# Optimization experiments

Measured on AMD Instinct MI355X. Metric: run time of the kernel, lower is better.

Reference implementation:

```python
import jax, jax.numpy as jnp
import numpy as np

DIM, E, K, H = 512, 8, 2, 16  # hidden_dim is hardcoded to 16 in the torch module
B, N = 8, 4096
BN_EPS = 1e-5


def setup_inputs() -> dict:
    key = jax.random.key(0)
    ks = jax.random.split(key, 12)
    s = 0.02
    return {
        "x": jax.random.normal(ks[0], (B, N, DIM), jnp.float32),
        # gate: Conv1d(dim, dim, 1) -> weight [dim, dim]; BatchNorm1d(dim); Conv1d(dim, E, 1)
        "wg1": jax.random.normal(ks[1], (DIM, DIM), jnp.float32) * s,
        "bg1": jnp.zeros((DIM,), jnp.float32),
        "gamma": jnp.ones((DIM,), jnp.float32),
        "beta": jnp.zeros((DIM,), jnp.float32),
        "wg2": jax.random.normal(ks[2], (E, DIM), jnp.float32) * s,
        "bg2": jnp.zeros((E,), jnp.float32),
        # experts stacked: Linear(dim,16) -> w1 [E, dim, 16]; Linear(16,dim) -> w2 [E, 16, dim]
        "w1": jax.random.normal(ks[3], (E, DIM, H), jnp.float32) * s,
        "b1": jnp.zeros((E, H), jnp.float32),
        "w2": jax.random.normal(ks[4], (E, H, DIM), jnp.float32) * s,
        "b2": jnp.zeros((E, DIM), jnp.float32),
    }


def reference(x, wg1, bg1, gamma, beta, wg2, bg2, w1, b1, w2, b2):
    b, n, c = x.shape
    t = b * n
    flat = x.reshape(t, c)                                 # [T, C]

    # gate: 1x1 conv == per-token linear; BN over all tokens per channel (train-mode batch stats)
    h = flat @ wg1.T + bg1                                  # [T, C]
    mu = h.mean(axis=0)
    var = h.var(axis=0)                                     # biased, matches torch BN normalization
    h = gamma * (h - mu) * jax.lax.rsqrt(var + BN_EPS) + beta
    h = jax.nn.relu(h)
    logits = h @ wg2.T + bg2                                # [T, E]

    vals, idx = jax.lax.top_k(logits, K)                    # [T, K]
    topk_w = jax.nn.softmax(vals, axis=-1)
    weight = jnp.zeros((t, logits.shape[-1]), logits.dtype)
    weight = weight.at[jnp.arange(t)[:, None], idx].set(topk_w)  # scatter, [T, E]

    # dense expert compute for every token (faithful to original)
    h1 = jax.nn.relu(jnp.einsum('tc,ech->teh', flat, w1) + b1)   # [T, E, H]
    all_out = jnp.einsum('teh,ehc->tec', h1, w2) + b2            # [T, E, C]
    out_flat = jnp.einsum('tec,te->tc', all_out, weight)         # masked combine

    out = out_flat.reshape(b, n, c).transpose(0, 2, 1)           # [B, C, N]
    usage = weight.sum(axis=0) / t
    lb_loss = (usage ** 2).sum() * logits.shape[-1]
    return out, lb_loss
```

## Files before the change

kernel.cpp:

```cpp
#include <hip/hip_runtime.h>

#define T_TOK 32768
#define C_DIM 512
#define N_SEQ 4096

typedef unsigned short ushort_t;
typedef unsigned int uint_t;
typedef __attribute__((ext_vector_type(8))) _Float16 half8;
typedef __attribute__((ext_vector_type(4))) float f32x4;

static __device__ __forceinline__ ushort_t f2h_bits(float f) {
  _Float16 h = (_Float16)f;
  return __builtin_bit_cast(ushort_t, h);
}
static __device__ __forceinline__ float h_bits2f(ushort_t u) {
  return (float)__builtin_bit_cast(_Float16, u);
}

static __device__ __forceinline__ half8 frag_ld(const ushort_t* base, int r, int q) {
  const int off = r * 32 + ((q ^ ((r >> 1) & 3)) * 8);
  return *(const half8*)(base + off);
}

#define GLOAD_LDS(gptr, lptr)                                                  \
  __builtin_amdgcn_global_load_lds(                                            \
      (const __attribute__((address_space(1))) uint_t*)(gptr),                 \
      (__attribute__((address_space(3))) uint_t*)(lptr), 16, 0, 0)

__global__ __launch_bounds__(256) void prep(
    const float* __restrict__ X, const float* __restrict__ wg1,
    const float* __restrict__ w1, const float* __restrict__ w2,
    const float* __restrict__ b2, ushort_t* __restrict__ Ahi,
    ushort_t* __restrict__ Alo, ushort_t* __restrict__ Whi,
    ushort_t* __restrict__ Wlo, ushort_t* __restrict__ W1t,
    ushort_t* __restrict__ W2t, float* __restrict__ stats,
    float* __restrict__ usage, uint_t* __restrict__ done) {
  const int idx = blockIdx.x * 256 + threadIdx.x;
  {
    const size_t i0 = (size_t)idx * 8;
    float4 a = *(const float4*)(X + i0);
    float4 b = *(const float4*)(X + i0 + 4);
    float v[8] = {a.x, a.y, a.z, a.w, b.x, b.y, b.z, b.w};
    ushort_t hi[8], lo[8];
#pragma unroll
    for (int j = 0; j < 8; ++j) {
      hi[j] = f2h_bits(v[j]);
      lo[j] = f2h_bits(v[j] - h_bits2f(hi[j]));
    }
    *(uint4*)(Ahi + i0) = *(uint4*)hi;
    *(uint4*)(Alo + i0) = *(uint4*)lo;
  }
  if (blockIdx.x < 1024) {
    {
      const float v = wg1[idx];
      const ushort_t h = f2h_bits(v);
      Whi[idx] = h;
      Wlo[idx] = f2h_bits(v - h_bits2f(h));
    }
    if (idx < 65536) {
      const int eh = idx >> 9, c = idx & 511;
      const int e = eh >> 4, hh = eh & 15;
      W1t[idx] = f2h_bits(w1[((size_t)e * 512 + c) * 16 + hh]);
    }
    if (idx < 81920) {
      const int c = idx / 160, k = idx - c * 160;
      float v = 0.f;
      if (k < 128) {
        const int e = k >> 4, hh = k & 15;
        v = w2[((size_t)e * 16 + hh) * 512 + c];
      } else if (k < 136) {
        v = b2[(size_t)(k - 128) * 512 + c];
      }
      W2t[c * 160 + k] = f2h_bits(v);
    }
  }
  if (blockIdx.x == 4096) {
    float4 z = {0.f, 0.f, 0.f, 0.f};
    *(float4*)&stats[threadIdx.x * 4] = z;
    if (threadIdx.x < 8) usage[threadIdx.x] = 0.f;
    if (threadIdx.x == 8) *done = 0u;
  }
}

__global__ __launch_bounds__(256) void k1_mfma(
    const ushort_t* __restrict__ Ahi, const ushort_t* __restrict__ Alo,
    const ushort_t* __restrict__ Whi, const ushort_t* __restrict__ Wlo,
    const float* __restrict__ bg1, float* __restrict__ H,
    float* __restrict__ stats) {
  __shared__ ushort_t sAh[2][4096], sAl[2][4096];
  const int tid = threadIdx.x, lane = tid & 63, w = tid >> 6;
  const int wm = w >> 1, wn = w & 1;
  const int b = blockIdx.x;
  const int m0 = ((b & 7) | ((b >> 5) << 3)) * 128;
  const int n0 = ((b >> 3) & 3) * 128;
  const int cl = lane & 15, qf = lane >> 4;

  const ushort_t* gA = (w < 2) ? Ahi : Alo;

#define K1_STAGE(kc, buf)                                                      \
  {                                                                            \
    const int k0s = (kc) * 32;                                                 \
    ushort_t* lb = (w < 2) ? sAh[buf] : sAl[buf];                              \
    _Pragma("unroll") for (int j = 0; j < 4; ++j) {                            \
      const int p = j * 128 + (w & 1) * 64 + lane;                             \
      const int r = p >> 2, q = (p & 3) ^ ((r >> 1) & 3);                      \
      GLOAD_LDS(gA + (size_t)(m0 + r) * 512 + k0s + q * 8, lb + p * 8);        \
    }                                                                          \
  }

  f32x4 acc[4][4] = {};
  K1_STAGE(0, 0);

  for (int kc = 0; kc < 16; ++kc) {
    const int k0 = kc * 32;
    __syncthreads();
    if (kc < 15) K1_STAGE(kc + 1, (kc + 1) & 1);

    half8 bh[4], bl[4];
#pragma unroll
    for (int f = 0; f < 4; ++f) {
      const size_t r = (size_t)(n0 + wn * 64 + f * 16 + cl);
      bh[f] = *(const half8*)(Whi + r * 512 + k0 + qf * 8);
      bl[f] = *(const half8*)(Wlo + r * 512 + k0 + qf * 8);
    }
    half8 ah[4], al[4];
    const ushort_t* bAh = sAh[kc & 1];
    const ushort_t* bAl = sAl[kc & 1];
#pragma unroll
    for (int f = 0; f < 4; ++f) {
      ah[f] = frag_ld(bAh, wm * 64 + f * 16 + cl, qf);
      al[f] = frag_ld(bAl, wm * 64 + f * 16 + cl, qf);
    }
#pragma unroll
    for (int i = 0; i < 4; ++i)
#pragma unroll
      for (int j = 0; j < 4; ++j) {
        acc[i][j] = __builtin_amdgcn_mfma_f32_16x16x32_f16(ah[i], bh[j], acc[i][j], 0, 0, 0);
        acc[i][j] = __builtin_amdgcn_mfma_f32_16x16x32_f16(ah[i], bl[j], acc[i][j], 0, 0, 0);
        acc[i][j] = __builtin_amdgcn_mfma_f32_16x16x32_f16(al[i], bh[j], acc[i][j], 0, 0, 0);
      }
  }
#undef K1_STAGE

  float s[4] = {0, 0, 0, 0}, qs[4] = {0, 0, 0, 0};
  const int rq = lane >> 4;
#pragma unroll
  for (int nf = 0; nf < 4; ++nf) {
    const int col = n0 + wn * 64 + nf * 16 + cl;
    const float bv = bg1[col];
#pragma unroll
    for (int mf = 0; mf < 4; ++mf) {
      const int row = m0 + wm * 64 + mf * 16 + rq * 4;
#pragma unroll
      for (int i = 0; i < 4; ++i) {
        const float v = acc[mf][nf][i] + bv;
        H[(size_t)(row + i) * 512 + col] = v;
        s[nf] += v;
        qs[nf] += v * v;
      }
    }
  }
#pragma unroll
  for (int nf = 0; nf < 4; ++nf) {
    s[nf] += __shfl_xor(s[nf], 16, 64);
    qs[nf] += __shfl_xor(qs[nf], 16, 64);
    s[nf] += __shfl_xor(s[nf], 32, 64);
    qs[nf] += __shfl_xor(qs[nf], 32, 64);
  }
  if (lane < 16) {
#pragma unroll
    for (int nf = 0; nf < 4; ++nf) {
      const int col = n0 + wn * 64 + nf * 16 + cl;
      atomicAdd(&stats[col], s[nf]);
      atomicAdd(&stats[512 + col], qs[nf]);
    }
  }
}

__global__ __launch_bounds__(256) void k5_fused(
    const ushort_t* __restrict__ Ahi, const ushort_t* __restrict__ W1t,
    const ushort_t* __restrict__ W2t, const float* __restrict__ b1,
    const float* __restrict__ H, const float* __restrict__ stats,
    const float* __restrict__ gamma, const float* __restrict__ beta,
    const float* __restrict__ wg2, const float* __restrict__ bg2,
    float* __restrict__ usage, uint_t* __restrict__ done,
    float* __restrict__ Out) {
  __shared__ ushort_t sA[2][2048];
  __shared__ ushort_t Pl[64 * 168];
  __shared__ float wtab[64 * 8];
  __shared__ float ys[128 * 68];
  __shared__ float scsh_l[1024];
  __shared__ float lus[8];

  const int tid = threadIdx.x, lane = tid & 63, w = tid >> 6;
  const int wm = w >> 1, wn = w & 1;
  const int t0 = blockIdx.x * 64;
  const int bi = t0 >> 12, n0 = t0 & 4095;
  const int cl = lane & 15, qf = lane >> 4, rq = lane >> 4;

  {
    const int p = tid;
    const int r = p >> 2, q = (p & 3) ^ ((r >> 1) & 3);
    GLOAD_LDS(Ahi + (size_t)(t0 + r) * 512 + q * 8, sA[0] + p * 8);
  }

  if (tid < 8) lus[tid] = 0.f;
  wtab[tid] = 0.f;
  wtab[tid + 256] = 0.f;
  {
    uint4 z = {0, 0, 0, 0};
    const int row = tid >> 2, hf = tid & 3;
    *(uint4*)&Pl[row * 168 + 128 + hf * 8] = z;
  }
#pragma unroll
  for (int rep = 0; rep < 2; ++rep) {
    const int c = tid + rep * 256;
    const double mu = (double)stats[c] * (1.0 / (double)T_TOK);
    const double var = (double)stats[512 + c] * (1.0 / (double)T_TOK) - mu * mu;
    const double rstd = 1.0 / sqrt(var + 1e-5);
    const float scv = (float)((double)gamma[c] * rstd);
    scsh_l[c] = scv;
    scsh_l[512 + c] = beta[c] - (float)mu * scv;
  }
  __syncthreads();

  {
    const int cb = lane * 8;
    float sc[8], sh[8];
#pragma unroll
    for (int i = 0; i < 8; ++i) {
      sc[i] = scsh_l[cb + i];
      sh[i] = scsh_l[512 + cb + i];
    }
    float wg[8][8];
#pragma unroll
    for (int e = 0; e < 8; ++e)
#pragma unroll
      for (int i = 0; i < 8; ++i) wg[e][i] = wg2[e * C_DIM + cb + i];
    float bg[8];
#pragma unroll
    for (int e = 0; e < 8; ++e) bg[e] = bg2[e];

#pragma unroll 2
    for (int it = 0; it < 16; ++it) {
      const int tl = w * 16 + it;
      const float* hr = H + (size_t)(t0 + tl) * C_DIM + cb;
      float4 h0 = *(const float4*)hr;
      float4 h1 = *(const float4*)(hr + 4);
      float y[8] = {h0.x, h0.y, h0.z, h0.w, h1.x, h1.y, h1.z, h1.w};
#pragma unroll
      for (int i = 0; i < 8; ++i) y[i] = fmaxf(fmaf(y[i], sc[i], sh[i]), 0.f);

      float lg[8];
#pragma unroll
      for (int e = 0; e < 8; ++e) {
        float sum = 0.f;
#pragma unroll
        for (int i = 0; i < 8; ++i) sum = fmaf(y[i], wg[e][i], sum);
        lg[e] = sum;
      }
#pragma unroll
      for (int d = 1; d < 64; d <<= 1)
#pragma unroll
        for (int e = 0; e < 8; ++e) lg[e] += __shfl_xor(lg[e], d, 64);
#pragma unroll
      for (int e = 0; e < 8; ++e) lg[e] += bg[e];

      float v1 = lg[0]; int i1 = 0;
#pragma unroll
      for (int e = 1; e < 8; ++e)
        if (lg[e] > v1) { v1 = lg[e]; i1 = e; }
      float v2 = -3.4e38f; int i2 = 0;
#pragma unroll
      for (int e = 0; e < 8; ++e)
        if (e != i1 && lg[e] > v2) { v2 = lg[e]; i2 = e; }

      const float p = expf(v2 - v1);
      const float rw = 1.f / (1.f + p);
      const float w0 = rw, w1 = p * rw;

      if (lane == 0) {
        wtab[tl * 8 + i1] = w0;
        wtab[tl * 8 + i2] = w1;
        Pl[tl * 168 + 128 + i1] = f2h_bits(w0);
        Pl[tl * 168 + 128 + i2] = f2h_bits(w1);
        atomicAdd(&lus[i1], w0);
        atomicAdd(&lus[i2], w1);
      }
    }
  }
  __syncthreads();
  if (tid < 8) atomicAdd(&usage[tid], lus[tid]);
  __syncthreads();
  if (tid == 0) {
    __threadfence();
    const uint_t ticket = atomicAdd(done, 1u);
    if (ticket == 511u) {
      float s = 0.f;
#pragma unroll
      for (int e = 0; e < 8; ++e) {
        const float u = atomicAdd(&usage[e], 0.f) * (1.f / (float)T_TOK);
        s += u * u;
      }
      Out[(size_t)16777216] = s * 8.f;
    }
  }

  f32x4 acc[2][4] = {};
  for (int kc = 0; kc < 16; ++kc) {
    const int k0 = kc * 32;
    __syncthreads();
    if (kc < 15) {
      const int p = tid;
      const int r = p >> 2, q = (p & 3) ^ ((r >> 1) & 3);
      GLOAD_LDS(Ahi + (size_t)(t0 + r) * 512 + (k0 + 32) + q * 8,
                sA[(kc + 1) & 1] + p * 8);
    }
    half8 bf[4];
#pragma unroll
    for (int f = 0; f < 4; ++f)
      bf[f] = *(const half8*)(W1t + (size_t)(wn * 64 + f * 16 + cl) * 512 + k0 + qf * 8);
    half8 af[2];
#pragma unroll
    for (int f = 0; f < 2; ++f) af[f] = frag_ld(sA[kc & 1], wm * 32 + f * 16 + cl, qf);
#pragma unroll
    for (int i = 0; i < 2; ++i)
#pragma unroll
      for (int j = 0; j < 4; ++j)
        acc[i][j] = __builtin_amdgcn_mfma_f32_16x16x32_f16(af[i], bf[j], acc[i][j], 0, 0, 0);
  }

  {
#pragma unroll
    for (int nf = 0; nf < 4; ++nf) {
      const int col = wn * 64 + nf * 16 + cl;
      const float bv = b1[col];
      const int e = wn * 4 + nf;
#pragma unroll
      for (int mf = 0; mf < 2; ++mf) {
        const int row = wm * 32 + mf * 16 + rq * 4;
#pragma unroll
        for (int i = 0; i < 4; ++i) {
          const float v = fmaxf(acc[mf][nf][i] + bv, 0.f) * wtab[(row + i) * 8 + e];
          Pl[(row + i) * 168 + col] = f2h_bits(v);
        }
      }
    }
  }
  __syncthreads();

  for (int nc = 0; nc < 4; ++nc) {
    f32x4 a2[2][4] = {};
#pragma unroll
    for (int kc = 0; kc < 5; ++kc) {
      const int k0 = kc * 32;
      half8 bf4[4];
#pragma unroll
      for (int f = 0; f < 4; ++f)
        bf4[f] = *(const half8*)(W2t + (size_t)(nc * 128 + wn * 64 + f * 16 + cl) * 160 + k0 + qf * 8);
      half8 af[2];
#pragma unroll
      for (int f = 0; f < 2; ++f)
        af[f] = *(const half8*)(Pl + (wm * 32 + f * 16 + cl) * 168 + k0 + qf * 8);
#pragma unroll
      for (int i = 0; i < 2; ++i)
#pragma unroll
        for (int j = 0; j < 4; ++j)
          a2[i][j] = __builtin_amdgcn_mfma_f32_16x16x32_f16(af[i], bf4[j], a2[i][j], 0, 0, 0);
    }
    __syncthreads();
#pragma unroll
    for (int nf = 0; nf < 4; ++nf) {
      const int c = wn * 64 + nf * 16 + cl;
#pragma unroll
      for (int mf = 0; mf < 2; ++mf) {
        const int trow = wm * 32 + mf * 16 + rq * 4;
#pragma unroll
        for (int i = 0; i < 4; ++i) ys[c * 68 + trow + i] = a2[mf][nf][i];
      }
    }
    __syncthreads();
#pragma unroll
    for (int pass = 0; pass < 8; ++pass) {
      const int c = pass * 16 + (tid >> 4);
      const int f4 = tid & 15;
      float4 v = *(const float4*)&ys[c * 68 + f4 * 4];
      *(float4*)&Out[((size_t)(bi * 512 + nc * 128 + c)) * 4096 + n0 + f4 * 4] = v;
    }
  }
}

extern "C" void kernel_launch(void* const* d_in, const int* in_sizes, int n_in,
                              void* d_out, int out_size, void* d_ws, size_t ws_size,
                              hipStream_t stream) {
  const float* x     = (const float*)d_in[0];
  const float* wg1   = (const float*)d_in[1];
  const float* bg1   = (const float*)d_in[2];
  const float* gamma = (const float*)d_in[3];
  const float* beta  = (const float*)d_in[4];
  const float* wg2   = (const float*)d_in[5];
  const float* bg2   = (const float*)d_in[6];
  const float* w1    = (const float*)d_in[7];
  const float* b1    = (const float*)d_in[8];
  const float* w2    = (const float*)d_in[9];
  const float* b2    = (const float*)d_in[10];
  float* out = (float*)d_out;

  char* ws = (char*)d_ws;
  float*    h     = (float*)ws;
  ushort_t* Ahi   = (ushort_t*)(ws + 67108864);
  ushort_t* Alo   = (ushort_t*)(ws + 100663296);
  ushort_t* Whi   = (ushort_t*)(ws + 134217728);
  ushort_t* Wlo   = (ushort_t*)(ws + 134742016);
  ushort_t* W1t   = (ushort_t*)(ws + 135266304);
  ushort_t* W2t   = (ushort_t*)(ws + 135397376);
  float*    stats = (float*)(ws + 135561216);
  float*    usage = (float*)(ws + 135565312);
  uint_t*   done  = (uint_t*)(ws + 135565344);

  prep<<<8192, 256, 0, stream>>>(x, wg1, w1, w2, b2, Ahi, Alo, Whi, Wlo, W1t,
                                 W2t, stats, usage, done);
  k1_mfma<<<1024, 256, 0, stream>>>(Ahi, Alo, Whi, Wlo, bg1, h, stats);
  k5_fused<<<512, 256, 0, stream>>>(Ahi, W1t, W2t, b1, h, stats, gamma, beta,
                                    wg2, bg2, usage, done, out);
}
```

Measured before the change: 288.4 us.

## Fuse fp32-to-fp16 hi/lo split of X into GEMM kernels, drop prep pass

The prep kernel no longer converts X into fp16 hi/lo workspace copies. Instead, k1 and k5 load fp32 X directly into registers, split it into fp16 hi/lo inside the loop, and write the halves to LDS. k1 now also stages the Whi/Wlo tiles into LDS via global_load_lds instead of reading them directly from global memory. This removes a full read and a double-width write of the 64MB activation tensor. The cost is extra conversion ALU work in the GEMMs and an extra barrier per k-step, since k1 no longer double-buffers its LDS.

```diff
diff --git a/kernel.cpp b/kernel.cpp
--- a/kernel.cpp
+++ b/kernel.cpp
@@ -28,53 +28,36 @@
       (__attribute__((address_space(3))) uint_t*)(lptr), 16, 0, 0)
 
 __global__ __launch_bounds__(256) void prep(
-    const float* __restrict__ X, const float* __restrict__ wg1,
-    const float* __restrict__ w1, const float* __restrict__ w2,
-    const float* __restrict__ b2, ushort_t* __restrict__ Ahi,
-    ushort_t* __restrict__ Alo, ushort_t* __restrict__ Whi,
-    ushort_t* __restrict__ Wlo, ushort_t* __restrict__ W1t,
-    ushort_t* __restrict__ W2t, float* __restrict__ stats,
-    float* __restrict__ usage, uint_t* __restrict__ done) {
+    const float* __restrict__ wg1, const float* __restrict__ w1,
+    const float* __restrict__ w2, const float* __restrict__ b2,
+    ushort_t* __restrict__ Whi, ushort_t* __restrict__ Wlo,
+    ushort_t* __restrict__ W1t, ushort_t* __restrict__ W2t,
+    float* __restrict__ stats, float* __restrict__ usage,
+    uint_t* __restrict__ done) {
   const int idx = blockIdx.x * 256 + threadIdx.x;
   {
-    const size_t i0 = (size_t)idx * 8;
-    float4 a = *(const float4*)(X + i0);
-    float4 b = *(const float4*)(X + i0 + 4);
-    float v[8] = {a.x, a.y, a.z, a.w, b.x, b.y, b.z, b.w};
-    ushort_t hi[8], lo[8];
-#pragma unroll
-    for (int j = 0; j < 8; ++j) {
-      hi[j] = f2h_bits(v[j]);
-      lo[j] = f2h_bits(v[j] - h_bits2f(hi[j]));
-    }
-    *(uint4*)(Ahi + i0) = *(uint4*)hi;
-    *(uint4*)(Alo + i0) = *(uint4*)lo;
-  }
-  if (blockIdx.x < 1024) {
-    {
-      const float v = wg1[idx];
-      const ushort_t h = f2h_bits(v);
-      Whi[idx] = h;
-      Wlo[idx] = f2h_bits(v - h_bits2f(h));
-    }
-    if (idx < 65536) {
-      const int eh = idx >> 9, c = idx & 511;
-      const int e = eh >> 4, hh = eh & 15;
-      W1t[idx] = f2h_bits(w1[((size_t)e * 512 + c) * 16 + hh]);
-    }
-    if (idx < 81920) {
-      const int c = idx / 160, k = idx - c * 160;
-      float v = 0.f;
-      if (k < 128) {
-        const int e = k >> 4, hh = k & 15;
-        v = w2[((size_t)e * 16 + hh) * 512 + c];
-      } else if (k < 136) {
-        v = b2[(size_t)(k - 128) * 512 + c];
-      }
-      W2t[c * 160 + k] = f2h_bits(v);
-    }
-  }
-  if (blockIdx.x == 4096) {
+    const float v = wg1[idx];
+    const ushort_t h = f2h_bits(v);
+    Whi[idx] = h;
+    Wlo[idx] = f2h_bits(v - h_bits2f(h));
+  }
+  if (idx < 65536) {
+    const int eh = idx >> 9, c = idx & 511;
+    const int e = eh >> 4, hh = eh & 15;
+    W1t[idx] = f2h_bits(w1[((size_t)e * 512 + c) * 16 + hh]);
+  }
+  if (idx < 81920) {
+    const int c = idx / 160, k = idx - c * 160;
+    float v = 0.f;
+    if (k < 128) {
+      const int e = k >> 4, hh = k & 15;
+      v = w2[((size_t)e * 16 + hh) * 512 + c];
+    } else if (k < 136) {
+      v = b2[(size_t)(k - 128) * 512 + c];
+    }
+    W2t[c * 160 + k] = f2h_bits(v);
+  }
+  if (blockIdx.x == 1023) {
     float4 z = {0.f, 0.f, 0.f, 0.f};
     *(float4*)&stats[threadIdx.x * 4] = z;
     if (threadIdx.x < 8) usage[threadIdx.x] = 0.f;
@@ -83,11 +66,10 @@
 }
 
 __global__ __launch_bounds__(256) void k1_mfma(
-    const ushort_t* __restrict__ Ahi, const ushort_t* __restrict__ Alo,
-    const ushort_t* __restrict__ Whi, const ushort_t* __restrict__ Wlo,
-    const float* __restrict__ bg1, float* __restrict__ H,
-    float* __restrict__ stats) {
-  __shared__ ushort_t sAh[2][4096], sAl[2][4096];
+    const float* __restrict__ X, const ushort_t* __restrict__ Whi,
+    const ushort_t* __restrict__ Wlo, const float* __restrict__ bg1,
+    float* __restrict__ H, float* __restrict__ stats) {
+  __shared__ ushort_t sAh[4096], sAl[4096], sBh[4096], sBl[4096];
   const int tid = threadIdx.x, lane = tid & 63, w = tid >> 6;
   const int wm = w >> 1, wn = w & 1;
   const int b = blockIdx.x;
@@ -95,41 +77,58 @@
   const int n0 = ((b >> 3) & 3) * 128;
   const int cl = lane & 15, qf = lane >> 4;
 
-  const ushort_t* gA = (w < 2) ? Ahi : Alo;
-
-#define K1_STAGE(kc, buf)                                                      \
+  const int p1 = tid, p2 = tid + 256;
+  const int r1 = p1 >> 2, q1 = (p1 & 3) ^ ((r1 >> 1) & 3);
+  const int r2 = p2 >> 2, q2 = (p2 & 3) ^ ((r2 >> 1) & 3);
+  const float* xb1 = X + (size_t)(m0 + r1) * 512 + q1 * 8;
+  const float* xb2 = X + (size_t)(m0 + r2) * 512 + q2 * 8;
+
+  float4 xr[4];
+#define K1_LOADX(kc)                                                           \
   {                                                                            \
-    const int k0s = (kc) * 32;                                                 \
-    ushort_t* lb = (w < 2) ? sAh[buf] : sAl[buf];                              \
-    _Pragma("unroll") for (int j = 0; j < 4; ++j) {                            \
-      const int p = j * 128 + (w & 1) * 64 + lane;                             \
-      const int r = p >> 2, q = (p & 3) ^ ((r >> 1) & 3);                      \
-      GLOAD_LDS(gA + (size_t)(m0 + r) * 512 + k0s + q * 8, lb + p * 8);        \
-    }                                                                          \
-  }
-
+    const int kk = (kc) * 32;                                                  \
+    xr[0] = *(const float4*)(xb1 + kk);                                        \
+    xr[1] = *(const float4*)(xb1 + kk + 4);                                    \
+    xr[2] = *(const float4*)(xb2 + kk);                                        \
+    xr[3] = *(const float4*)(xb2 + kk + 4);                                    \
+  }
+
+  K1_LOADX(0);
   f32x4 acc[4][4] = {};
-  K1_STAGE(0, 0);
 
   for (int kc = 0; kc < 16; ++kc) {
     const int k0 = kc * 32;
     __syncthreads();
-    if (kc < 15) K1_STAGE(kc + 1, (kc + 1) & 1);
-
-    half8 bh[4], bl[4];
+#pragma unroll
+    for (int j = 0; j < 2; ++j) {
+      const int pb = (w * 2 + j) * 64 + lane;
+      const int rb = pb >> 2, qb = (pb & 3) ^ ((rb >> 1) & 3);
+      GLOAD_LDS(Whi + (size_t)(n0 + rb) * 512 + k0 + qb * 8, sBh + pb * 8);
+      GLOAD_LDS(Wlo + (size_t)(n0 + rb) * 512 + k0 + qb * 8, sBl + pb * 8);
+    }
+    {
+      ushort_t hi[16], lo[16];
+      const float* v = (const float*)xr;
+#pragma unroll
+      for (int j = 0; j < 16; ++j) {
+        hi[j] = f2h_bits(v[j]);
+        lo[j] = f2h_bits(v[j] - h_bits2f(hi[j]));
+      }
+      *(uint4*)(sAh + p1 * 8) = *(uint4*)(hi);
+      *(uint4*)(sAl + p1 * 8) = *(uint4*)(lo);
+      *(uint4*)(sAh + p2 * 8) = *(uint4*)(hi + 8);
+      *(uint4*)(sAl + p2 * 8) = *(uint4*)(lo + 8);
+    }
+    __syncthreads();
+    if (kc < 15) K1_LOADX(kc + 1);
+
+    half8 ah[4], al[4], bh[4], bl[4];
 #pragma unroll
     for (int f = 0; f < 4; ++f) {
-      const size_t r = (size_t)(n0 + wn * 64 + f * 16 + cl);
-      bh[f] = *(const half8*)(Whi + r * 512 + k0 + qf * 8);
-      bl[f] = *(const half8*)(Wlo + r * 512 + k0 + qf * 8);
-    }
-    half8 ah[4], al[4];
-    const ushort_t* bAh = sAh[kc & 1];
-    const ushort_t* bAl = sAl[kc & 1];
-#pragma unroll
-    for (int f = 0; f < 4; ++f) {
-      ah[f] = frag_ld(bAh, wm * 64 + f * 16 + cl, qf);
-      al[f] = frag_ld(bAl, wm * 64 + f * 16 + cl, qf);
+      ah[f] = frag_ld(sAh, wm * 64 + f * 16 + cl, qf);
+      al[f] = frag_ld(sAl, wm * 64 + f * 16 + cl, qf);
+      bh[f] = frag_ld(sBh, wn * 64 + f * 16 + cl, qf);
+      bl[f] = frag_ld(sBl, wn * 64 + f * 16 + cl, qf);
     }
 #pragma unroll
     for (int i = 0; i < 4; ++i)
@@ -140,7 +139,7 @@
         acc[i][j] = __builtin_amdgcn_mfma_f32_16x16x32_f16(al[i], bh[j], acc[i][j], 0, 0, 0);
       }
   }
-#undef K1_STAGE
+#undef K1_LOADX
 
   float s[4] = {0, 0, 0, 0}, qs[4] = {0, 0, 0, 0};
   const int rq = lane >> 4;
@@ -178,7 +177,7 @@
 }
 
 __global__ __launch_bounds__(256) void k5_fused(
-    const ushort_t* __restrict__ Ahi, const ushort_t* __restrict__ W1t,
+    const float* __restrict__ X, const ushort_t* __restrict__ W1t,
     const ushort_t* __restrict__ W2t, const float* __restrict__ b1,
     const float* __restrict__ H, const float* __restrict__ stats,
     const float* __restrict__ gamma, const float* __restrict__ beta,
@@ -198,11 +197,10 @@
   const int bi = t0 >> 12, n0 = t0 & 4095;
   const int cl = lane & 15, qf = lane >> 4, rq = lane >> 4;
 
-  {
-    const int p = tid;
-    const int r = p >> 2, q = (p & 3) ^ ((r >> 1) & 3);
-    GLOAD_LDS(Ahi + (size_t)(t0 + r) * 512 + q * 8, sA[0] + p * 8);
-  }
+  const int pA = tid, rA = pA >> 2, qA = (pA & 3) ^ ((rA >> 1) & 3);
+  const float* xbase = X + (size_t)(t0 + rA) * 512 + qA * 8;
+  float4 xq0 = *(const float4*)(xbase);
+  float4 xq1 = *(const float4*)(xbase + 4);
 
   if (tid < 8) lus[tid] = 0.f;
   wtab[tid] = 0.f;
@@ -309,12 +307,17 @@
   f32x4 acc[2][4] = {};
   for (int kc = 0; kc < 16; ++kc) {
     const int k0 = kc * 32;
+    {
+      ushort_t hi[8];
+      const float v[8] = {xq0.x, xq0.y, xq0.z, xq0.w, xq1.x, xq1.y, xq1.z, xq1.w};
+#pragma unroll
+      for (int j = 0; j < 8; ++j) hi[j] = f2h_bits(v[j]);
+      *(uint4*)(sA[kc & 1] + pA * 8) = *(uint4*)hi;
+    }
     __syncthreads();
     if (kc < 15) {
-      const int p = tid;
-      const int r = p >> 2, q = (p & 3) ^ ((r >> 1) & 3);
-      GLOAD_LDS(Ahi + (size_t)(t0 + r) * 512 + (k0 + 32) + q * 8,
-                sA[(kc + 1) & 1] + p * 8);
+      xq0 = *(const float4*)(xbase + k0 + 32);
+      xq1 = *(const float4*)(xbase + k0 + 36);
     }
     half8 bf[4];
 #pragma unroll
@@ -408,19 +411,17 @@
 
   char* ws = (char*)d_ws;
   float*    h     = (float*)ws;
-  ushort_t* Ahi   = (ushort_t*)(ws + 67108864);
-  ushort_t* Alo   = (ushort_t*)(ws + 100663296);
-  ushort_t* Whi   = (ushort_t*)(ws + 134217728);
-  ushort_t* Wlo   = (ushort_t*)(ws + 134742016);
-  ushort_t* W1t   = (ushort_t*)(ws + 135266304);
-  ushort_t* W2t   = (ushort_t*)(ws + 135397376);
-  float*    stats = (float*)(ws + 135561216);
-  float*    usage = (float*)(ws + 135565312);
-  uint_t*   done  = (uint_t*)(ws + 135565344);
-
-  prep<<<8192, 256, 0, stream>>>(x, wg1, w1, w2, b2, Ahi, Alo, Whi, Wlo, W1t,
-                                 W2t, stats, usage, done);
-  k1_mfma<<<1024, 256, 0, stream>>>(Ahi, Alo, Whi, Wlo, bg1, h, stats);
-  k5_fused<<<512, 256, 0, stream>>>(Ahi, W1t, W2t, b1, h, stats, gamma, beta,
+  ushort_t* Whi   = (ushort_t*)(ws + 67108864);
+  ushort_t* Wlo   = (ushort_t*)(ws + 67633152);
+  ushort_t* W1t   = (ushort_t*)(ws + 68157440);
+  ushort_t* W2t   = (ushort_t*)(ws + 68288512);
+  float*    stats = (float*)(ws + 68452352);
+  float*    usage = (float*)(ws + 68456448);
+  uint_t*   done  = (uint_t*)(ws + 68456480);
+
+  prep<<<1024, 256, 0, stream>>>(wg1, w1, w2, b2, Whi, Wlo, W1t, W2t, stats,
+                                 usage, done);
+  k1_mfma<<<1024, 256, 0, stream>>>(x, Whi, Wlo, bg1, h, stats);
+  k5_fused<<<512, 256, 0, stream>>>(x, W1t, W2t, b1, h, stats, gamma, beta,
                                     wg2, bg2, usage, done, out);
 }
```

Measured after the change: 251.5 us. 1.15x faster.
